# Kernel tuning notes

Hardware: AMD Instinct MI355X
Metric: run time of the kernel (lower is better)

## Reference

```python
import jax, jax.numpy as jnp
import numpy as np

TAU = 0.07      # temperature from __init__ default
TOP_K = 10      # hardcoded k in torch.topk
DIAG_FILL = -10.0
TOP_SIM_VAL = 0.75


def setup_inputs() -> dict:
    key = jax.random.key(0)
    k1, k2 = jax.random.split(key)
    z1 = jax.random.normal(k1, (4096, 512), dtype=jnp.float32)
    z2 = jax.random.normal(k2, (4096, 512), dtype=jnp.float32)
    return {"z1": z1, "z2": z2}


def reference(z1, z2):
    # AllGather is identity on a single device; grad_scaling=False.
    z = jnp.concatenate([z1, z2], axis=0)                      # [n, d]
    # F.normalize(dim=1): divide by L2 norm (eps-clamped)
    norm = jnp.maximum(jnp.linalg.norm(z, axis=1, keepdims=True), 1e-12)
    z = z / norm
    n = z.shape[0]
    half = n // 2

    # labels: ones at offsets +n/2 and -n/2 == identity rolled by n/2
    labels = jnp.roll(jnp.eye(n, dtype=z.dtype), half, axis=1)  # [n, n]

    sim = z @ z.T                                               # [n, n]

    # top_k_based_on_cos_sim branch: softmax of raw sim (diag still present)
    cos_sim = jax.nn.softmax(sim, axis=1)
    idx = jnp.arange(n)
    # branch mask: 0 on same-half blocks, 1 on cross-half blocks
    mask = ((idx[:, None] < half) ^ (idx[None, :] < half)).astype(z.dtype)
    cos_sim = cos_sim * mask
    _, top_idx = jax.lax.top_k(cos_sim, TOP_K)                  # [n, K]
    top_sim = jnp.zeros((n, n), dtype=z.dtype).at[idx[:, None], top_idx].set(TOP_SIM_VAL)
    labels = jnp.maximum(labels, top_sim)

    # fill diagonal with -10, scale by temperature, row log-softmax
    sim = sim.at[idx, idx].set(DIAG_FILL) / TAU
    logp = jax.nn.log_softmax(sim, axis=1)
    loss = -jnp.sum(logp * labels) / n
    return loss
```

## Files before the change

kernel.cpp:

```cpp
#include <hip/hip_runtime.h>
#include <hip/hip_bf16.h>
#include <stdint.h>

#define N_TOTAL 8192
#define HALF_N  4096
#define DIM     512
#define INV_TAU (1.0f/0.07f)
#define EXP2_SCALE  4.5398160046388386f
#define SIM_FROM_VE 0.0485203026391962f

typedef __attribute__((ext_vector_type(4))) int   i32x4;

#define AS1 __attribute__((address_space(1)))
#define AS3 __attribute__((address_space(3)))

__device__ __forceinline__ uint32_t umax32(uint32_t a, uint32_t b) { return a > b ? a : b; }
__device__ __forceinline__ uint32_t umin32(uint32_t a, uint32_t b) { return a < b ? a : b; }

#define DPP_SHR_F32(x, ctrl) \
    __int_as_float(__builtin_amdgcn_update_dpp(0, __float_as_int(x), (ctrl), 0xf, 0xf, true))
#define DPP_SHR_U32(x, ctrl) \
    ((uint32_t)__builtin_amdgcn_update_dpp(0, (int)(x), (ctrl), 0xf, 0xf, true))

#define TOP2_DPP_STEP(t1, t2, ctrl) do {                                           \
    uint32_t o1_ = DPP_SHR_U32(t1, ctrl);                                          \
    uint32_t o2_ = DPP_SHR_U32(t2, ctrl);                                          \
    uint32_t mn_ = umin32(t1, o1_);                                                \
    t1 = umax32(t1, o1_);                                                          \
    o2_ = umax32(t2, o2_);                                                         \
    t2 = umax32(mn_, o2_);                                                         \
} while (0)

__device__ __forceinline__ float decode_key(uint32_t key)
{
    ushort h = (key & 0x8000u) ? (ushort)(key ^ 0x8000u) : (ushort)(key ^ 0xFFFFu);
    return (float)(*(_Float16*)&h);
}

__global__ __launch_bounds__(256) void norm_kernel(const float* __restrict__ z1,
                                                   const float* __restrict__ z2,
                                                   char* __restrict__ zq,
                                                   float* __restrict__ inv_e,
                                                   float* __restrict__ rowsum)
{
    if (threadIdx.x < 4) rowsum[blockIdx.x * 4 + threadIdx.x] = 0.f;

    int row  = blockIdx.x * 4 + (threadIdx.x >> 6);
    int lane = threadIdx.x & 63;
    const float* src = (row < HALF_N) ? (z1 + (size_t)row * DIM)
                                      : (z2 + (size_t)(row - HALF_N) * DIM);
    const float4* p = (const float4*)src;
    float4 a = p[lane * 2];
    float4 b = p[lane * 2 + 1];
    float ss = a.x*a.x + a.y*a.y + a.z*a.z + a.w*a.w
             + b.x*b.x + b.y*b.y + b.z*b.z + b.w*b.w;
#pragma unroll
    for (int o = 1; o < 64; o <<= 1) ss += __shfl_xor(ss, o);
    float sc = 127.0f / fmaxf(sqrtf(ss), 1e-12f);

    float v[8] = {a.x*sc, a.y*sc, a.z*sc, a.w*sc, b.x*sc, b.y*sc, b.z*sc, b.w*sc};
    char c8[8];
    int qq = 0;
#pragma unroll
    for (int j = 0; j < 8; j++) {
        int qi = (int)rintf(v[j]);
        qq += qi * qi;
        c8[j] = (char)qi;
    }
#pragma unroll
    for (int o = 1; o < 64; o <<= 1) qq += __shfl_xor(qq, o);
    if (lane == 0) inv_e[row] = EXP2_SCALE / sqrtf(fmaxf((float)qq, 1.0f));

    *(uint2*)(zq + (size_t)row * DIM + lane * 8) = *(const uint2*)c8;
}

__global__ __launch_bounds__(256, 4) void gemm_kernel(const char* __restrict__ zq,
                                                      const float* __restrict__ inv_e,
                                                      float* __restrict__ rowsum,
                                                      uint2* __restrict__ partial,
                                                      float* __restrict__ pos_sim)
{
    int orig = blockIdx.x;
    int bid  = (orig & 7) * 260 + (orig >> 3);

    int by = (int)(64.5f - sqrtf(4160.25f - 2.0f * (float)bid));
    int off = 64 * by - (by * (by - 1)) / 2;
    if (off > bid) { --by; off = 64 * by - (by * (by - 1)) / 2; }
    else {
        int offn = 64 * (by + 1) - ((by + 1) * by) / 2;
        if (offn <= bid) { ++by; off = offn; }
    }
    int bx = by + (bid - off);

    const int brow = by * 128;
    const int bcol = bx * 128;

    __shared__ char As[2][128 * 64];
    __shared__ char Bs[2][128 * 64];

    const int t    = threadIdx.x;
    const int w    = t >> 6;
    const int lane = t & 63;
    const int wr   = w >> 1, wc = w & 1;

    i32x4 acc[4][4] = {};

    const int c0 = t, c1 = 256 + t;
    const int r0 = c0 >> 2, r1 = c1 >> 2;
    const int q0 = (c0 & 3) ^ ((r0 >> 1) & 3);
    const int q1 = (c1 & 3) ^ ((r1 >> 1) & 3);
    const size_t gaA0 = (size_t)(brow + r0) * DIM + q0 * 16;
    const size_t gaA1 = (size_t)(brow + r1) * DIM + q1 * 16;
    const size_t gaB0 = (size_t)(bcol + r0) * DIM + q0 * 16;
    const size_t gaB1 = (size_t)(bcol + r1) * DIM + q1 * 16;
    const int l0 = (w * 64) * 16;
    const int l1 = (256 + w * 64) * 16;

#define STAGE(buf, ko) do {                                                        \
    __builtin_amdgcn_global_load_lds((const AS1 uint32_t*)(zq + gaA0 + (ko)),      \
        (AS3 uint32_t*)((char*)As[buf] + l0), 16, 0, 0);                           \
    __builtin_amdgcn_global_load_lds((const AS1 uint32_t*)(zq + gaA1 + (ko)),      \
        (AS3 uint32_t*)((char*)As[buf] + l1), 16, 0, 0);                           \
    __builtin_amdgcn_global_load_lds((const AS1 uint32_t*)(zq + gaB0 + (ko)),      \
        (AS3 uint32_t*)((char*)Bs[buf] + l0), 16, 0, 0);                           \
    __builtin_amdgcn_global_load_lds((const AS1 uint32_t*)(zq + gaB1 + (ko)),      \
        (AS3 uint32_t*)((char*)Bs[buf] + l1), 16, 0, 0);                           \
} while (0)

    STAGE(0, 0);
    __syncthreads();

    int cur = 0;
    for (int kt = 0; kt < DIM / 64; ++kt) {
        if (kt + 1 < DIM / 64) STAGE(cur ^ 1, (kt + 1) * 64);

        i32x4 av[4], bv[4];
#pragma unroll
        for (int m = 0; m < 4; m++) {
            int ro = wr * 64 + m * 16 + (lane & 15);
            int s  = (lane >> 4) ^ ((ro >> 1) & 3);
            av[m] = *(const i32x4*)(As[cur] + ro * 64 + s * 16);
        }
#pragma unroll
        for (int n = 0; n < 4; n++) {
            int ro = wc * 64 + n * 16 + (lane & 15);
            int s  = (lane >> 4) ^ ((ro >> 1) & 3);
            bv[n] = *(const i32x4*)(Bs[cur] + ro * 64 + s * 16);
        }
#pragma unroll
        for (int m = 0; m < 4; m++)
#pragma unroll
            for (int n = 0; n < 4; n++)
                acc[m][n] = __builtin_amdgcn_mfma_i32_16x16x64_i8(av[m], bv[n], acc[m][n], 0, 0, 0);

        __syncthreads();
        cur ^= 1;
    }
#undef STAGE

    const bool is_cross = (brow < HALF_N) && (bcol >= HALF_N);
    const bool off_diag = (bx != by);

    float invc[4];
#pragma unroll
    for (int n = 0; n < 4; n++)
        invc[n] = inv_e[bcol + wc * 64 + n * 16 + (lane & 15)];

    float invr_[4][4];
#pragma unroll
    for (int m = 0; m < 4; m++) {
        float4 v4 = *(const float4*)&inv_e[brow + wr * 64 + m * 16 + ((lane >> 4) << 2)];
        invr_[m][0] = v4.x; invr_[m][1] = v4.y; invr_[m][2] = v4.z; invr_[m][3] = v4.w;
    }

    float    cs0[4] = {0,0,0,0}, cs1[4] = {0,0,0,0};
    uint32_t s1a[4] = {0,0,0,0}, s2a[4] = {0,0,0,0};
    uint32_t s1b[4] = {0,0,0,0}, s2b[4] = {0,0,0,0};

#pragma unroll
    for (int m = 0; m < 4; m++) {
#pragma unroll
        for (int r = 0; r < 4; r++) {
            int grow = brow + wr * 64 + m * 16 + ((lane >> 4) << 2) + r;
            float invr = invr_[m][r];
            float rs = 0.f;
            uint32_t t1 = 0u, t2 = 0u;
#pragma unroll
            for (int n = 0; n < 4; n++) {
                int gcol = bcol + wc * 64 + n * 16 + (lane & 15);
                float ve = (float)acc[m][n][r] * (invr * invc[n]);
                float e  = (grow == gcol) ? 0.f : __builtin_exp2f(ve);
                rs += e;
                if (m < 2) cs0[n] += e; else cs1[n] += e;
                if (is_cross) {
                    float v = ve * SIM_FROM_VE;
                    int cidx = gcol - HALF_N;
                    ushort h;
                    *(_Float16*)&h = (_Float16)v;
                    uint32_t key = ((uint32_t)(ushort)(h ^ (ushort)((ushort)((short)h >> 15) | 0x8000))) << 16;
                    uint32_t xr = key | (uint32_t)(4095 - cidx);
                    uint32_t mn = umin32(t1, xr);
                    t1 = umax32(t1, xr);
                    t2 = umax32(t2, mn);
                    uint32_t xc = key | (uint32_t)(4095 - grow);
                    if (m < 2) {
                        mn = umin32(s1a[n], xc); s1a[n] = umax32(s1a[n], xc); s2a[n] = umax32(s2a[n], mn);
                    } else {
                        mn = umin32(s1b[n], xc); s1b[n] = umax32(s1b[n], xc); s2b[n] = umax32(s2b[n], mn);
                    }
                    if (cidx == grow) { pos_sim[grow] = v; pos_sim[gcol] = v; }
                }
            }
            rs += DPP_SHR_F32(rs, 0x111);
            rs += DPP_SHR_F32(rs, 0x112);
            rs += DPP_SHR_F32(rs, 0x114);
            rs += DPP_SHR_F32(rs, 0x118);
            if ((lane & 15) == 15) atomicAdd(&rowsum[grow], rs);

            if (is_cross) {
                TOP2_DPP_STEP(t1, t2, 0x111);
                TOP2_DPP_STEP(t1, t2, 0x112);
                TOP2_DPP_STEP(t1, t2, 0x114);
                TOP2_DPP_STEP(t1, t2, 0x118);
                if ((lane & 15) == 15)
                    partial[((size_t)grow << 6) + (bx - 32) * 2 + wc] = make_uint2(t1, t2);
            }
        }
    }

    if (off_diag) {
#pragma unroll
        for (int n = 0; n < 4; n++) {
            float c = cs0[n] + cs1[n];
            c += __shfl_xor(c, 16);
            c += __shfl_xor(c, 32);
            uint32_t a1 = umax32(s1a[n], s1b[n]);
            uint32_t a2 = umax32(umin32(s1a[n], s1b[n]), umax32(s2a[n], s2b[n]));
            if (is_cross) {
#pragma unroll
                for (int o = 16; o < 64; o <<= 1) {
                    uint32_t o1 = __shfl_xor(a1, o);
                    uint32_t o2 = __shfl_xor(a2, o);
                    uint32_t nt2 = umax32(umin32(a1, o1), umax32(a2, o2));
                    a1 = umax32(a1, o1);
                    a2 = nt2;
                }
            }
            if (lane < 16) {
                int gcol = bcol + wc * 64 + n * 16 + lane;
                atomicAdd(&rowsum[gcol], c);
                if (is_cross)
                    partial[((size_t)gcol << 6) + by * 2 + wr] = make_uint2(a1, a2);
            }
        }
    }
}

__global__ __launch_bounds__(256) void topk_loss_kernel(const uint2* __restrict__ partial,
                                                        const float* __restrict__ pos_sim,
                                                        const float* __restrict__ rowsum,
                                                        float* __restrict__ contrib)
{
    int i    = blockIdx.x * 4 + (threadIdx.x >> 6);
    int lane = threadIdx.x & 63;

    uint2 p = partial[((size_t)i << 6) + lane];
    uint32_t t1 = p.x, t2 = p.y;

    int posidx = i & (HALF_N - 1);
    float S10 = 0.f; int posflag = 0;
#pragma unroll
    for (int tc = 0; tc < 10; tc++) {
        uint32_t b = umax32(t1, t2);
#pragma unroll
        for (int o = 32; o; o >>= 1)
            b = umax32(b, __shfl_xor(b, o));
        bool w1 = (b == t1);
        bool w2 = (b == t2);
        t1 = w1 ? t2 : t1;
        t2 = (w1 | w2) ? 0u : t2;

        int idx = 4095 - (int)(b & 0xFFFFu);
        S10 += decode_key(b >> 16);
        posflag |= (idx == posidx) ? 1 : 0;
    }

    if (lane == 0) {
        float ps  = pos_sim[i];
        float lse = logf(rowsum[i]);
        float L   = 1.0f + 0.75f * (10 - posflag);
        float sll = INV_TAU * (ps + 0.75f * (S10 - posflag * ps));
        contrib[i] = L * lse - sll;
    }
}

__global__ __launch_bounds__(256) void reduce_kernel(const float* __restrict__ contrib,
                                                     float* __restrict__ out)
{
    int t = threadIdx.x;
    float s = 0.f;
    for (int j = t; j < N_TOTAL; j += 256) s += contrib[j];
#pragma unroll
    for (int o = 1; o < 64; o <<= 1) s += __shfl_xor(s, o);
    __shared__ float wsum[4];
    if ((t & 63) == 0) wsum[t >> 6] = s;
    __syncthreads();
    if (t == 0) out[0] = (wsum[0] + wsum[1] + wsum[2] + wsum[3]) * (1.0f / N_TOTAL);
}

extern "C" void kernel_launch(void* const* d_in, const int* in_sizes, int n_in,
                              void* d_out, int out_size, void* d_ws, size_t ws_size,
                              hipStream_t stream)
{
    const float* z1 = (const float*)d_in[0];
    const float* z2 = (const float*)d_in[1];
    float* out = (float*)d_out;

    char* ws = (char*)d_ws;
    char*   zq      = ws;
    float*  rowsum  = (float*)(ws + 4194304);
    float*  pos_sim = (float*)(ws + 4227072);
    float*  inv_e   = (float*)(ws + 4259840);
    uint2*  partial = (uint2*)(ws + 4292608);
    float*  contrib = (float*)(ws + 8486912);

    norm_kernel<<<N_TOTAL / 4, 256, 0, stream>>>(z1, z2, zq, inv_e, rowsum);
    gemm_kernel<<<2080, 256, 0, stream>>>(zq, inv_e, rowsum, partial, pos_sim);
    topk_loss_kernel<<<N_TOTAL / 4, 256, 0, stream>>>(partial, pos_sim, rowsum, contrib);
    reduce_kernel<<<1, 256, 0, stream>>>(contrib, out);
}
```

Before: 81.78 us.

## Fuse final reduction into top-k kernel and reorder GEMM tile schedule

Removes the separate single-block reduce launch by having the last-finishing top-k block, detected through an atomic counter that the norm kernel resets, perform the final sum. It also changes the GEMM block-to-tile mapping so that cross-half tiles are scheduled first, followed by the two within-half triangles, grouped per chunk. This saves one kernel launch and may improve load balance or cache locality, at the cost of an atomic counter and fences in every top-k block.

```diff
diff --git a/kernel.cpp b/kernel.cpp
--- a/kernel.cpp
+++ b/kernel.cpp
@@ -41,9 +41,11 @@
                                                    const float* __restrict__ z2,
                                                    char* __restrict__ zq,
                                                    float* __restrict__ inv_e,
-                                                   float* __restrict__ rowsum)
+                                                   float* __restrict__ rowsum,
+                                                   int* __restrict__ counter)
 {
     if (threadIdx.x < 4) rowsum[blockIdx.x * 4 + threadIdx.x] = 0.f;
+    if (blockIdx.x == 0 && threadIdx.x == 0) atomicExch(counter, 0);
 
     int row  = blockIdx.x * 4 + (threadIdx.x >> 6);
     int lane = threadIdx.x & 63;
@@ -80,17 +82,29 @@
                                                       uint2* __restrict__ partial,
                                                       float* __restrict__ pos_sim)
 {
-    int orig = blockIdx.x;
-    int bid  = (orig & 7) * 260 + (orig >> 3);
-
-    int by = (int)(64.5f - sqrtf(4160.25f - 2.0f * (float)bid));
-    int off = 64 * by - (by * (by - 1)) / 2;
-    if (off > bid) { --by; off = 64 * by - (by * (by - 1)) / 2; }
-    else {
-        int offn = 64 * (by + 1) - ((by + 1) * by) / 2;
-        if (offn <= bid) { ++by; off = offn; }
-    }
-    int bx = by + (bid - off);
+    const int chunk = blockIdx.x & 7;
+    const int pos   = blockIdx.x >> 3;
+    int by, bx;
+    const bool is_cross = (pos < 128);
+    if (is_cross) {
+        int k = chunk * 128 + pos;
+        by = k >> 5;
+        bx = 32 + (k & 31);
+    } else {
+        int k2 = chunk * 132 + (pos - 128);
+        int half = (k2 >= 528) ? 1 : 0;
+        int tt = k2 - 528 * half;
+        int ty = (int)(32.5f - sqrtf(1056.25f - 2.0f * (float)tt));
+        int o  = 32 * ty - (ty * (ty - 1)) / 2;
+        if (o > tt) { --ty; o = 32 * ty - (ty * (ty - 1)) / 2; }
+        else {
+            int on = 32 * (ty + 1) - ((ty + 1) * ty) / 2;
+            if (on <= tt) { ++ty; o = on; }
+        }
+        int tx = ty + (tt - o);
+        by = ty + (half << 5);
+        bx = tx + (half << 5);
+    }
 
     const int brow = by * 128;
     const int bcol = bx * 128;
@@ -158,7 +172,6 @@
     }
 #undef STAGE
 
-    const bool is_cross = (brow < HALF_N) && (bcol >= HALF_N);
     const bool off_diag = (bx != by);
 
     float invc[4];
@@ -259,8 +272,13 @@
 __global__ __launch_bounds__(256) void topk_loss_kernel(const uint2* __restrict__ partial,
                                                         const float* __restrict__ pos_sim,
                                                         const float* __restrict__ rowsum,
-                                                        float* __restrict__ contrib)
-{
+                                                        float* __restrict__ contrib,
+                                                        int* __restrict__ counter,
+                                                        float* __restrict__ out)
+{
+    __shared__ int slast;
+    __shared__ float wsum[4];
+
     int i    = blockIdx.x * 4 + (threadIdx.x >> 6);
     int lane = threadIdx.x & 63;
 
@@ -292,20 +310,25 @@
         float sll = INV_TAU * (ps + 0.75f * (S10 - posflag * ps));
         contrib[i] = L * lse - sll;
     }
-}
-
-__global__ __launch_bounds__(256) void reduce_kernel(const float* __restrict__ contrib,
-                                                     float* __restrict__ out)
-{
-    int t = threadIdx.x;
-    float s = 0.f;
-    for (int j = t; j < N_TOTAL; j += 256) s += contrib[j];
-#pragma unroll
-    for (int o = 1; o < 64; o <<= 1) s += __shfl_xor(s, o);
-    __shared__ float wsum[4];
-    if ((t & 63) == 0) wsum[t >> 6] = s;
+
     __syncthreads();
-    if (t == 0) out[0] = (wsum[0] + wsum[1] + wsum[2] + wsum[3]) * (1.0f / N_TOTAL);
+    if (threadIdx.x == 0) {
+        __threadfence();
+        int old = atomicAdd(counter, 1);
+        slast = (old == (int)gridDim.x - 1);
+    }
+    __syncthreads();
+    if (slast) {
+        __threadfence();
+        int tt = threadIdx.x;
+        float s = 0.f;
+        for (int j = tt; j < N_TOTAL; j += 256) s += contrib[j];
+#pragma unroll
+        for (int o = 1; o < 64; o <<= 1) s += __shfl_xor(s, o);
+        if ((tt & 63) == 0) wsum[tt >> 6] = s;
+        __syncthreads();
+        if (tt == 0) out[0] = (wsum[0] + wsum[1] + wsum[2] + wsum[3]) * (1.0f / N_TOTAL);
+    }
 }
 
 extern "C" void kernel_launch(void* const* d_in, const int* in_sizes, int n_in,
@@ -323,9 +346,9 @@
     float*  inv_e   = (float*)(ws + 4259840);
     uint2*  partial = (uint2*)(ws + 4292608);
     float*  contrib = (float*)(ws + 8486912);
-
-    norm_kernel<<<N_TOTAL / 4, 256, 0, stream>>>(z1, z2, zq, inv_e, rowsum);
+    int*    counter = (int*)(ws + 8519680);
+
+    norm_kernel<<<N_TOTAL / 4, 256, 0, stream>>>(z1, z2, zq, inv_e, rowsum, counter);
     gemm_kernel<<<2080, 256, 0, stream>>>(zq, inv_e, rowsum, partial, pos_sim);
-    topk_loss_kernel<<<N_TOTAL / 4, 256, 0, stream>>>(partial, pos_sim, rowsum, contrib);
-    reduce_kernel<<<1, 256, 0, stream>>>(contrib, out);
-}
+    topk_loss_kernel<<<N_TOTAL / 4, 256, 0, stream>>>(partial, pos_sim, rowsum, contrib, counter, out);
+}
```

Measured after the change: 113.7 us (median of 4 runs). 1.39x slower.
